# Optimization experiments

Hardware: AMD Instinct MI355X
Metric: run time of the kernel (lower is better)

The kernel has to match this reference:

```python
import jax, jax.numpy as jnp
import numpy as np

N, E, H, R = 50000, 800000, 256, 8
LN_EPS = 1e-5


def setup_inputs() -> dict:
    key = jax.random.key(0)
    ks = jax.random.split(key, 6)
    node_states = jax.random.normal(ks[0], (N, H), dtype=jnp.float32)
    edge_index = jax.random.randint(ks[1], (2, E), 0, N, dtype=jnp.int64)
    edge_type_ids = jax.random.randint(ks[2], (E,), 0, R, dtype=jnp.int64)
    scale = 1.0 / np.sqrt(H)
    W_rel = jax.random.normal(ks[3], (R, H, H), dtype=jnp.float32) * scale
    W_root = jax.random.normal(ks[4], (H, H), dtype=jnp.float32) * scale
    bias = jnp.zeros((H,), dtype=jnp.float32)
    ln_gamma = jnp.ones((H,), dtype=jnp.float32)
    ln_beta = jnp.zeros((H,), dtype=jnp.float32)
    return {
        "node_states": node_states,
        "edge_index": edge_index,
        "edge_type_ids": edge_type_ids,
        "W_rel": W_rel,
        "W_root": W_root,
        "bias": bias,
        "ln_gamma": ln_gamma,
        "ln_beta": ln_beta,
    }


def _rgcn_layer(node_states, edge_index, edge_type_ids, W_rel, W_root, bias, ln_gamma, ln_beta):
    n, h = node_states.shape
    r = W_rel.shape[0]
    src, dst = edge_index[0], edge_index[1]
    # Per-(dst, relation) MEAN of source features (PyG RGCNConv default aggr='mean').
    seg = dst * r + edge_type_ids  # composite segment id in [0, N*R)
    msgs = node_states[src]  # [E, H] gather
    sums = jax.ops.segment_sum(msgs, seg, num_segments=n * r).reshape(n, r, h)
    counts = jax.ops.segment_sum(jnp.ones((src.shape[0],), node_states.dtype), seg,
                                 num_segments=n * r).reshape(n, r, 1)
    mean = sums / jnp.maximum(counts, 1.0)  # zero-edge buckets stay 0
    # Relation-specific linear transforms applied to aggregated means, then root + bias.
    agg = jnp.einsum('nrh,rho->no', mean, W_rel)
    conv = agg + node_states @ W_root + bias
    # Exact (erf-based) GELU to match torch.nn.functional.gelu default.
    updated = jax.nn.gelu(conv, approximate=False)
    # Dropout is identity in eval mode.
    x = updated + node_states  # residual
    mu = jnp.mean(x, axis=-1, keepdims=True)
    var = jnp.mean(jnp.square(x - mu), axis=-1, keepdims=True)
    return ln_gamma * (x - mu) * jax.lax.rsqrt(var + LN_EPS) + ln_beta


def reference(node_states, edge_index, edge_type_ids, W_rel, W_root, bias, ln_gamma, ln_beta):
    return _rgcn_layer(node_states, edge_index, edge_type_ids, W_rel, W_root, bias, ln_gamma, ln_beta)
```

## Files before the change

### kernel.cpp

```cpp
#include <hip/hip_runtime.h>
#include <cstdint>
#include <cstddef>

#define N_NODES 50000
#define N_EDGES 800000
#define HDIM    256
#define NREL    8
#define NSEG    (N_NODES * NREL)
#define KDIM    (NREL * HDIM + HDIM)
#define LN_EPSF 1e-5f

#define SCAN_CHUNK 1024
#define SCAN_NB    ((NSEG + SCAN_CHUNK - 1) / SCAN_CHUNK)

using short8  = __attribute__((ext_vector_type(8))) short;
using ushort8 = __attribute__((ext_vector_type(8))) unsigned short;
using float4v = __attribute__((ext_vector_type(4))) float;

static __device__ __forceinline__ unsigned short f2bf(float f) {
    union { float f; uint32_t i; } v; v.f = f;
    uint32_t r = v.i + 0x7FFFu + ((v.i >> 16) & 1u);
    return (unsigned short)(r >> 16);
}
static __device__ __forceinline__ float bf2f(unsigned short u) {
    union { uint32_t i; float f; } v; v.i = ((uint32_t)u) << 16; return v.f;
}

__global__ __launch_bounds__(256) void k_cast(const float* __restrict__ ns,
                                              unsigned short* __restrict__ ns16) {
    int idx = blockIdx.x * blockDim.x + threadIdx.x;
    if (idx >= N_NODES * HDIM / 8) return;
    const float4v* nsv = (const float4v*)ns;
    float4v v0 = nsv[idx * 2], v1 = nsv[idx * 2 + 1];
    ushort8 o;
    o[0] = f2bf(v0[0]); o[1] = f2bf(v0[1]); o[2] = f2bf(v0[2]); o[3] = f2bf(v0[3]);
    o[4] = f2bf(v1[0]); o[5] = f2bf(v1[1]); o[6] = f2bf(v1[2]); o[7] = f2bf(v1[3]);
    *(ushort8*)&ns16[(size_t)idx * 8] = o;
}

__global__ void k_count(const int* __restrict__ ei, const int* __restrict__ et,
                        int* __restrict__ cnt) {
    int e = blockIdx.x * blockDim.x + threadIdx.x;
    if (e >= N_EDGES) return;
    int dst = ei[N_EDGES + e];
    int rel = et[e];
    atomicAdd(&cnt[dst * NREL + rel], 1);
}

__global__ __launch_bounds__(256) void k_scan1(const int* __restrict__ cnt,
                                               int* __restrict__ bsum) {
    int b = blockIdx.x, t = threadIdx.x;
    int idx = b * SCAN_CHUNK + t * 4;
    int4 v = {0, 0, 0, 0};
    if (idx + 3 < NSEG) v = *(const int4*)&cnt[idx];
    else {
        #pragma unroll
        for (int j = 0; j < 4; ++j) if (idx + j < NSEG) ((int*)&v)[j] = cnt[idx + j];
    }
    int s = v.x + v.y + v.z + v.w;
    #pragma unroll
    for (int o = 32; o > 0; o >>= 1) s += __shfl_xor(s, o, 64);
    __shared__ int ls[4];
    if ((t & 63) == 0) ls[t >> 6] = s;
    __syncthreads();
    if (t == 0) bsum[b] = ls[0] + ls[1] + ls[2] + ls[3];
}

__global__ __launch_bounds__(512) void k_scan2(const int* __restrict__ bsum,
                                               int* __restrict__ boff) {
    __shared__ int s[512];
    int t = threadIdx.x;
    int v = (t < SCAN_NB) ? bsum[t] : 0;
    s[t] = v;
    __syncthreads();
    for (int d = 1; d < 512; d <<= 1) {
        int x = (t >= d) ? s[t - d] : 0;
        __syncthreads();
        s[t] += x;
        __syncthreads();
    }
    if (t < SCAN_NB) boff[t] = s[t] - v;
}

__global__ __launch_bounds__(256) void k_scan3(const int* __restrict__ cnt,
                                               const int* __restrict__ boff,
                                               int* __restrict__ off) {
    int b = blockIdx.x, t = threadIdx.x;
    int idx = b * SCAN_CHUNK + t * 4;
    int4 v = {0, 0, 0, 0};
    if (idx + 3 < NSEG) v = *(const int4*)&cnt[idx];
    else {
        #pragma unroll
        for (int j = 0; j < 4; ++j) if (idx + j < NSEG) ((int*)&v)[j] = cnt[idx + j];
    }
    int s = v.x + v.y + v.z + v.w;
    __shared__ int ls[256];
    ls[t] = s;
    __syncthreads();
    for (int d = 1; d < 256; d <<= 1) {
        int x = (t >= d) ? ls[t - d] : 0;
        __syncthreads();
        ls[t] += x;
        __syncthreads();
    }
    int run = boff[b] + ls[t] - s;
    int4 w;
    w.x = run; run += v.x;
    w.y = run; run += v.y;
    w.z = run; run += v.z;
    w.w = run;
    if (idx + 3 < NSEG) *(int4*)&off[idx] = w;
    else {
        #pragma unroll
        for (int j = 0; j < 4; ++j) if (idx + j < NSEG) off[idx + j] = ((int*)&w)[j];
    }
    if (b == 0 && t == 0) off[NSEG] = N_EDGES;
}

__global__ void k_scatter(const int* __restrict__ ei, const int* __restrict__ et,
                          const int* __restrict__ off, int* __restrict__ cursor,
                          int* __restrict__ srcs) {
    int e = blockIdx.x * blockDim.x + threadIdx.x;
    if (e >= N_EDGES) return;
    int src = ei[e];
    int dst = ei[N_EDGES + e];
    int rel = et[e];
    int seg = dst * NREL + rel;
    int pos = off[seg] + atomicAdd(&cursor[seg], 1);
    srcs[pos] = src;
}

__global__ __launch_bounds__(256) void k_aggregate(const unsigned short* __restrict__ ns16,
                                                   const int* __restrict__ off,
                                                   const int* __restrict__ srcs,
                                                   unsigned short* __restrict__ Afull) {
    int n = blockIdx.x, t = threadIdx.x;
    int g = t >> 5;
    int i = t & 31;
    int seg = n * NREL + g;
    int e0 = off[seg], e1 = off[seg + 1];
    int cnt = e1 - e0;
    int cs = cnt < 32 ? cnt : 32;
    int my_src = (i < cs) ? srcs[e0 + i] : 0;

    const ushort8* nsv = (const ushort8*)ns16;
    float acc[8] = {0.f, 0.f, 0.f, 0.f, 0.f, 0.f, 0.f, 0.f};

    for (int k = 0; k < cs; ++k) {
        int src = __shfl(my_src, k, 32);
        ushort8 v = nsv[(size_t)src * 32 + i];
        #pragma unroll
        for (int j = 0; j < 8; ++j) acc[j] += bf2f(v[j]);
    }
    for (int e = e0 + 32; e < e1; ++e) {
        int src = srcs[e];
        ushort8 v = nsv[(size_t)src * 32 + i];
        #pragma unroll
        for (int j = 0; j < 8; ++j) acc[j] += bf2f(v[j]);
    }

    float inv = (cnt > 0) ? 1.0f / (float)cnt : 0.0f;
    ushort8 wv;
    #pragma unroll
    for (int j = 0; j < 8; ++j) wv[j] = f2bf(acc[j] * inv);
    __builtin_nontemporal_store(wv,
        (ushort8*)&Afull[(size_t)n * KDIM + g * HDIM + i * 8]);

    if (g == 0) {
        ushort8 rv = nsv[(size_t)n * 32 + i];
        __builtin_nontemporal_store(rv,
            (ushort8*)&Afull[(size_t)n * KDIM + NREL * HDIM + i * 8]);
    }
}

__global__ void k_buildB(const float* __restrict__ Wrel, const float* __restrict__ Wroot,
                         unsigned short* __restrict__ Bt) {
    int idx = blockIdx.x * blockDim.x + threadIdx.x;
    if (idx >= HDIM * KDIM) return;
    int j = idx / KDIM;
    int k = idx % KDIM;
    float v;
    if (k < NREL * HDIM) {
        int r = k >> 8, h = k & 255;
        v = Wrel[((size_t)r * HDIM + h) * HDIM + j];
    } else {
        int h = k - NREL * HDIM;
        v = Wroot[(size_t)h * HDIM + j];
    }
    Bt[idx] = f2bf(v);
}

#define BM 128
#define BN 256
#define BK 64
#define NITER (KDIM / BK)

__global__ __launch_bounds__(256, 2) void k_gemm(const unsigned short* __restrict__ A,
                                                 const unsigned short* __restrict__ Bt,
                                                 const float* __restrict__ ns,
                                                 const float* __restrict__ bias,
                                                 const float* __restrict__ gamma,
                                                 const float* __restrict__ beta,
                                                 float* __restrict__ out, int M) {
    __shared__ __align__(16) unsigned short As[BM * BK];
    __shared__ __align__(16) unsigned short Bs[BN * BK];
    __shared__ float s1buf[BM][2], s2buf[BM][2];

    int tid  = threadIdx.x;
    int lane = tid & 63;
    int wid  = tid >> 6;
    int wm   = wid >> 1, wn = wid & 1;
    int brow = blockIdx.x * BM;

    float4v acc[4][8] = {};

    const char* Ab = (const char*)A;
    const char* Bb = (const char*)Bt;
    const size_t rstride = (size_t)KDIM * 2;

    for (int kt = 0; kt < KDIM; kt += BK) {
        #pragma unroll
        for (int i = 0; i < 4; ++i) {
            int linear = i * 4096 + tid * 16;
            int row  = linear >> 7;
            int slot = (linear >> 4) & 7;
            int kb   = (slot ^ (row & 7)) * 16;
            int ra = brow + row; if (ra > M - 1) ra = M - 1;
            const char* ga = Ab + (size_t)ra * rstride + (size_t)(kt * 2 + kb);
            __builtin_amdgcn_global_load_lds(
                (const __attribute__((address_space(1))) void*)ga,
                (__attribute__((address_space(3))) void*)((char*)As + linear),
                16, 0, 0);
        }
        #pragma unroll
        for (int i = 0; i < 8; ++i) {
            int linear = i * 4096 + tid * 16;
            int row  = linear >> 7;
            int slot = (linear >> 4) & 7;
            int kb   = (slot ^ (row & 7)) * 16;
            const char* gb = Bb + (size_t)row * rstride + (size_t)(kt * 2 + kb);
            __builtin_amdgcn_global_load_lds(
                (const __attribute__((address_space(1))) void*)gb,
                (__attribute__((address_space(3))) void*)((char*)Bs + linear),
                16, 0, 0);
        }
        __syncthreads();

        #pragma unroll
        for (int h = 0; h < 2; ++h) {
            short8 a[4], b[8];
            int s0 = h * 4 + (lane >> 4);
            #pragma unroll
            for (int m = 0; m < 4; ++m) {
                int r = wm * 64 + m * 16 + (lane & 15);
                a[m] = *(const short8*)((const char*)As + r * 128 + ((s0 ^ (r & 7)) * 16));
            }
            #pragma unroll
            for (int n = 0; n < 8; ++n) {
                int r = wn * 128 + n * 16 + (lane & 15);
                b[n] = *(const short8*)((const char*)Bs + r * 128 + ((s0 ^ (r & 7)) * 16));
            }
            #pragma unroll
            for (int m = 0; m < 4; ++m)
                #pragma unroll
                for (int n = 0; n < 8; ++n)
                    acc[m][n] = __builtin_amdgcn_mfma_f32_16x16x32_bf16(a[m], b[n], acc[m][n], 0, 0, 0);
        }
        __syncthreads();
    }

    int cols[8];
    float bias_v[8];
    #pragma unroll
    for (int n = 0; n < 8; ++n) {
        cols[n] = wn * 128 + n * 16 + (lane & 15);
        bias_v[n] = bias[cols[n]];
    }

    #pragma unroll
    for (int m = 0; m < 4; ++m) {
        #pragma unroll
        for (int q = 0; q < 4; ++q) {
            int lr = wm * 64 + m * 16 + (lane >> 4) * 4 + q;
            int r  = brow + lr;
            float s1 = 0.f, s2 = 0.f;
            #pragma unroll
            for (int n = 0; n < 8; ++n) {
                float conv = acc[m][n][q] + bias_v[n];
                float g = 0.5f * conv * (1.0f + erff(conv * 0.70710678118654752f));
                float resid = (r < M) ? ns[(size_t)r * HDIM + cols[n]] : 0.f;
                float x = g + resid;
                acc[m][n][q] = x;
                s1 += x; s2 += x * x;
            }
            #pragma unroll
            for (int o = 8; o > 0; o >>= 1) {
                s1 += __shfl_xor(s1, o, 64);
                s2 += __shfl_xor(s2, o, 64);
            }
            if ((lane & 15) == 0) { s1buf[lr][wn] = s1; s2buf[lr][wn] = s2; }
        }
    }
    __syncthreads();

    float gam[8], bet[8];
    #pragma unroll
    for (int n = 0; n < 8; ++n) { gam[n] = gamma[cols[n]]; bet[n] = beta[cols[n]]; }

    #pragma unroll
    for (int m = 0; m < 4; ++m) {
        #pragma unroll
        for (int q = 0; q < 4; ++q) {
            int lr = wm * 64 + m * 16 + (lane >> 4) * 4 + q;
            int r  = brow + lr;
            float t1 = s1buf[lr][0] + s1buf[lr][1];
            float t2 = s2buf[lr][0] + s2buf[lr][1];
            float mu  = t1 * (1.0f / HDIM);
            float var = t2 * (1.0f / HDIM) - mu * mu;
            float rstd = rsqrtf(var + LN_EPSF);
            if (r < M) {
                #pragma unroll
                for (int n = 0; n < 8; ++n) {
                    float x = acc[m][n][q];
                    out[(size_t)r * HDIM + cols[n]] = gam[n] * (x - mu) * rstd + bet[n];
                }
            }
        }
    }
}

extern "C" void kernel_launch(void* const* d_in, const int* in_sizes, int n_in,
                              void* d_out, int out_size, void* d_ws, size_t ws_size,
                              hipStream_t stream) {
    const float* ns    = (const float*)d_in[0];
    const int*   ei    = (const int*)d_in[1];
    const int*   et    = (const int*)d_in[2];
    const float* Wrel  = (const float*)d_in[3];
    const float* Wroot = (const float*)d_in[4];
    const float* bias  = (const float*)d_in[5];
    const float* gamma = (const float*)d_in[6];
    const float* beta  = (const float*)d_in[7];
    float* out = (float*)d_out;

    char* w = (char*)d_ws;
    auto take = [&](size_t bytes) -> char* {
        char* p = w; w += (bytes + 255) & ~(size_t)255; return p;
    };
    int* cnt              = (int*)take((size_t)NSEG * 4);
    int* segoff           = (int*)take((size_t)(NSEG + 1) * 4);
    int* cursor           = (int*)take((size_t)NSEG * 4);
    int* srcs             = (int*)take((size_t)N_EDGES * 4);
    int* bsum             = (int*)take((size_t)SCAN_NB * 4);
    int* boff             = (int*)take((size_t)SCAN_NB * 4);
    unsigned short* Afull = (unsigned short*)take((size_t)N_NODES * KDIM * 2);
    unsigned short* Bt    = (unsigned short*)take((size_t)HDIM * KDIM * 2);
    unsigned short* ns16  = (unsigned short*)take((size_t)N_NODES * HDIM * 2);

    hipMemsetAsync(cnt, 0, (size_t)NSEG * 4, stream);
    hipMemsetAsync(cursor, 0, (size_t)NSEG * 4, stream);

    k_cast<<<(N_NODES * HDIM / 8 + 255) / 256, 256, 0, stream>>>(ns, ns16);
    k_count<<<(N_EDGES + 255) / 256, 256, 0, stream>>>(ei, et, cnt);
    k_scan1<<<SCAN_NB, 256, 0, stream>>>(cnt, bsum);
    k_scan2<<<1, 512, 0, stream>>>(bsum, boff);
    k_scan3<<<SCAN_NB, 256, 0, stream>>>(cnt, boff, segoff);
    k_scatter<<<(N_EDGES + 255) / 256, 256, 0, stream>>>(ei, et, segoff, cursor, srcs);
    k_aggregate<<<N_NODES, 256, 0, stream>>>(ns16, segoff, srcs, Afull);
    k_buildB<<<(HDIM * KDIM + 255) / 256, 256, 0, stream>>>(Wrel, Wroot, Bt);

    dim3 gg((N_NODES + BM - 1) / BM, 1);
    k_gemm<<<gg, 256, 0, stream>>>(Afull, Bt, ns, bias, gamma, beta, out, N_NODES);
}
```

Measured before the change: 308.6 us.

## Use 8-wave GEMM blocks and tiled transpose for weight packing

The fused GEMM now runs 512 threads per block in a 2x4 wave grid, so each wave owns a 64x64 output tile instead of 64x128. That halves the per-wave accumulator registers, and the LayerNorm reduction now combines four column partials. The weight packing kernel now transposes through a padded shared-memory tile, so both the reads and the writes are coalesced. The cost is more waves contending for the same LDS tiles and a lower MFMA-to-LDS-read ratio per wave.

```diff
diff --git a/kernel.cpp b/kernel.cpp
--- a/kernel.cpp
+++ b/kernel.cpp
@@ -173,21 +173,36 @@
     }
 }
 
-__global__ void k_buildB(const float* __restrict__ Wrel, const float* __restrict__ Wroot,
-                         unsigned short* __restrict__ Bt) {
-    int idx = blockIdx.x * blockDim.x + threadIdx.x;
-    if (idx >= HDIM * KDIM) return;
-    int j = idx / KDIM;
-    int k = idx % KDIM;
-    float v;
-    if (k < NREL * HDIM) {
-        int r = k >> 8, h = k & 255;
-        v = Wrel[((size_t)r * HDIM + h) * HDIM + j];
-    } else {
-        int h = k - NREL * HDIM;
-        v = Wroot[(size_t)h * HDIM + j];
-    }
-    Bt[idx] = f2bf(v);
+__global__ __launch_bounds__(256) void k_buildB(const float* __restrict__ Wrel,
+                                                const float* __restrict__ Wroot,
+                                                unsigned short* __restrict__ Bt) {
+    __shared__ unsigned short tile[64][66];
+    int k0 = blockIdx.x * 64;
+    int j0 = blockIdx.y * 64;
+    int t = threadIdx.x;
+
+    #pragma unroll
+    for (int p = 0; p < 16; ++p) {
+        int idx = p * 256 + t;
+        int kk = idx >> 6, jj = idx & 63;
+        int k = k0 + kk;
+        float v;
+        if (k < NREL * HDIM) {
+            int r = k >> 8, h = k & 255;
+            v = Wrel[((size_t)r * HDIM + h) * HDIM + (j0 + jj)];
+        } else {
+            int h = k - NREL * HDIM;
+            v = Wroot[(size_t)h * HDIM + (j0 + jj)];
+        }
+        tile[kk][jj] = f2bf(v);
+    }
+    __syncthreads();
+    #pragma unroll
+    for (int p = 0; p < 16; ++p) {
+        int idx = p * 256 + t;
+        int jj = idx >> 6, kk = idx & 63;
+        Bt[(size_t)(j0 + jj) * KDIM + (k0 + kk)] = tile[kk][jj];
+    }
 }
 
 #define BM 128
@@ -195,7 +210,7 @@
 #define BK 64
 #define NITER (KDIM / BK)
 
-__global__ __launch_bounds__(256, 2) void k_gemm(const unsigned short* __restrict__ A,
+__global__ __launch_bounds__(512, 4) void k_gemm(const unsigned short* __restrict__ A,
                                                  const unsigned short* __restrict__ Bt,
                                                  const float* __restrict__ ns,
                                                  const float* __restrict__ bias,
@@ -204,15 +219,15 @@
                                                  float* __restrict__ out, int M) {
     __shared__ __align__(16) unsigned short As[BM * BK];
     __shared__ __align__(16) unsigned short Bs[BN * BK];
-    __shared__ float s1buf[BM][2], s2buf[BM][2];
+    __shared__ float s1buf[BM][4], s2buf[BM][4];
 
     int tid  = threadIdx.x;
     int lane = tid & 63;
     int wid  = tid >> 6;
-    int wm   = wid >> 1, wn = wid & 1;
+    int wm   = wid >> 2, wn = wid & 3;
     int brow = blockIdx.x * BM;
 
-    float4v acc[4][8] = {};
+    float4v acc[4][4] = {};
 
     const char* Ab = (const char*)A;
     const char* Bb = (const char*)Bt;
@@ -220,8 +235,8 @@
 
     for (int kt = 0; kt < KDIM; kt += BK) {
         #pragma unroll
-        for (int i = 0; i < 4; ++i) {
-            int linear = i * 4096 + tid * 16;
+        for (int i = 0; i < 2; ++i) {
+            int linear = i * 8192 + tid * 16;
             int row  = linear >> 7;
             int slot = (linear >> 4) & 7;
             int kb   = (slot ^ (row & 7)) * 16;
@@ -233,8 +248,8 @@
                 16, 0, 0);
         }
         #pragma unroll
-        for (int i = 0; i < 8; ++i) {
-            int linear = i * 4096 + tid * 16;
+        for (int i = 0; i < 4; ++i) {
+            int linear = i * 8192 + tid * 16;
             int row  = linear >> 7;
             int slot = (linear >> 4) & 7;
             int kb   = (slot ^ (row & 7)) * 16;
@@ -248,7 +263,7 @@
 
         #pragma unroll
         for (int h = 0; h < 2; ++h) {
-            short8 a[4], b[8];
+            short8 a[4], b[4];
             int s0 = h * 4 + (lane >> 4);
             #pragma unroll
             for (int m = 0; m < 4; ++m) {
@@ -256,24 +271,24 @@
                 a[m] = *(const short8*)((const char*)As + r * 128 + ((s0 ^ (r & 7)) * 16));
             }
             #pragma unroll
-            for (int n = 0; n < 8; ++n) {
-                int r = wn * 128 + n * 16 + (lane & 15);
+            for (int n = 0; n < 4; ++n) {
+                int r = wn * 64 + n * 16 + (lane & 15);
                 b[n] = *(const short8*)((const char*)Bs + r * 128 + ((s0 ^ (r & 7)) * 16));
             }
             #pragma unroll
             for (int m = 0; m < 4; ++m)
                 #pragma unroll
-                for (int n = 0; n < 8; ++n)
+                for (int n = 0; n < 4; ++n)
                     acc[m][n] = __builtin_amdgcn_mfma_f32_16x16x32_bf16(a[m], b[n], acc[m][n], 0, 0, 0);
         }
         __syncthreads();
     }
 
-    int cols[8];
-    float bias_v[8];
-    #pragma unroll
-    for (int n = 0; n < 8; ++n) {
-        cols[n] = wn * 128 + n * 16 + (lane & 15);
+    int cols[4];
+    float bias_v[4];
+    #pragma unroll
+    for (int n = 0; n < 4; ++n) {
+        cols[n] = wn * 64 + n * 16 + (lane & 15);
         bias_v[n] = bias[cols[n]];
     }
 
@@ -285,7 +300,7 @@
             int r  = brow + lr;
             float s1 = 0.f, s2 = 0.f;
             #pragma unroll
-            for (int n = 0; n < 8; ++n) {
+            for (int n = 0; n < 4; ++n) {
                 float conv = acc[m][n][q] + bias_v[n];
                 float g = 0.5f * conv * (1.0f + erff(conv * 0.70710678118654752f));
                 float resid = (r < M) ? ns[(size_t)r * HDIM + cols[n]] : 0.f;
@@ -303,9 +318,9 @@
     }
     __syncthreads();
 
-    float gam[8], bet[8];
-    #pragma unroll
-    for (int n = 0; n < 8; ++n) { gam[n] = gamma[cols[n]]; bet[n] = beta[cols[n]]; }
+    float gam[4], bet[4];
+    #pragma unroll
+    for (int n = 0; n < 4; ++n) { gam[n] = gamma[cols[n]]; bet[n] = beta[cols[n]]; }
 
     #pragma unroll
     for (int m = 0; m < 4; ++m) {
@@ -313,14 +328,14 @@
         for (int q = 0; q < 4; ++q) {
             int lr = wm * 64 + m * 16 + (lane >> 4) * 4 + q;
             int r  = brow + lr;
-            float t1 = s1buf[lr][0] + s1buf[lr][1];
-            float t2 = s2buf[lr][0] + s2buf[lr][1];
+            float t1 = s1buf[lr][0] + s1buf[lr][1] + s1buf[lr][2] + s1buf[lr][3];
+            float t2 = s2buf[lr][0] + s2buf[lr][1] + s2buf[lr][2] + s2buf[lr][3];
             float mu  = t1 * (1.0f / HDIM);
             float var = t2 * (1.0f / HDIM) - mu * mu;
             float rstd = rsqrtf(var + LN_EPSF);
             if (r < M) {
                 #pragma unroll
-                for (int n = 0; n < 8; ++n) {
+                for (int n = 0; n < 4; ++n) {
                     float x = acc[m][n][q];
                     out[(size_t)r * HDIM + cols[n]] = gam[n] * (x - mu) * rstd + bet[n];
                 }
@@ -366,8 +381,9 @@
     k_scan3<<<SCAN_NB, 256, 0, stream>>>(cnt, boff, segoff);
     k_scatter<<<(N_EDGES + 255) / 256, 256, 0, stream>>>(ei, et, segoff, cursor, srcs);
     k_aggregate<<<N_NODES, 256, 0, stream>>>(ns16, segoff, srcs, Afull);
-    k_buildB<<<(HDIM * KDIM + 255) / 256, 256, 0, stream>>>(Wrel, Wroot, Bt);
+    dim3 gb(KDIM / 64, HDIM / 64);
+    k_buildB<<<gb, 256, 0, stream>>>(Wrel, Wroot, Bt);
 
     dim3 gg((N_NODES + BM - 1) / BM, 1);
-    k_gemm<<<gg, 256, 0, stream>>>(Afull, Bt, ns, bias, gamma, beta, out, N_NODES);
-}
+    k_gemm<<<gg, 512, 0, stream>>>(Afull, Bt, ns, bias, gamma, beta, out, N_NODES);
+}
```

New measurement: 305.6 us. About the same (-1.0%).
